# Kernel optimization log

Measured on AMD Instinct MI355X. Metric: run time of the kernel, lower is better.

Reference implementation:

```python
import jax, jax.numpy as jnp
import numpy as np

B, H, W, C = 4, 64, 64, 256
CP = C // 2  # downsize_factor = 2

def setup_inputs() -> dict:
    key = jax.random.key(0)
    ks = jax.random.split(key, 5)
    s = 1.0 / np.sqrt(C)
    return {
        "x": jax.random.normal(ks[0], (B, H, W, C), dtype=jnp.float32),
        "Wk": jax.random.normal(ks[1], (C, CP), dtype=jnp.float32) * s,
        "bk": jnp.zeros((CP,), dtype=jnp.float32),
        "Wq": jax.random.normal(ks[2], (C, CP), dtype=jnp.float32) * s,
        "bq": jnp.zeros((CP,), dtype=jnp.float32),
        "Wv": jax.random.normal(ks[3], (C, CP), dtype=jnp.float32) * s,
        "bv": jnp.zeros((CP,), dtype=jnp.float32),
        "Ws": jax.random.normal(ks[4], (C, CP), dtype=jnp.float32) * s,
        "bs": jnp.zeros((CP,), dtype=jnp.float32),
    }

def reference(x, Wk, bk, Wq, bq, Wv, bv, Ws, bs):
    b, h, w, c = x.shape
    n = h * w
    xf = x.reshape(b, n, c)  # 1x1 conv == per-pixel matmul
    K = xf @ Wk + bk  # [b, n, c']
    Q = xf @ Wq + bq  # [b, n, c']
    V = xf @ Wv + bv  # [b, n, c']
    # Keras Dot(axes=(2,1))([K, Q^T]) -> scores = K @ Q^T (no 1/sqrt(d) scaling)
    scores = jnp.einsum('bnc,bmc->bnm', K, Q)
    attn = jax.nn.softmax(scores, axis=-1)
    out = jnp.einsum('bnm,bmc->bnc', attn, V)  # [b, n, c']
    shortcut = xf @ Ws + bs  # downsize_factor > 1 path
    return (out + shortcut).reshape(b, h, w, out.shape[-1])
```

## Files before the change

kernel.cpp:

```cpp
#include <hip/hip_runtime.h>
#include <math.h>

typedef unsigned short u16;
typedef __attribute__((ext_vector_type(8))) _Float16 half8;
typedef __attribute__((ext_vector_type(4))) float    f32x4;

#define BATCH 4
#define NPB   4096
#define BN    16384
#define CC    256
#define D     128
#define LOG2E 1.44269504088896f
#define THR   8.0f

#if __has_builtin(__builtin_amdgcn_exp2f)
#define EXP2(x) __builtin_amdgcn_exp2f(x)
#else
#define EXP2(x) exp2f(x)
#endif

template<int CTRL>
__device__ __forceinline__ float dpp_mov(float x) {
    return __builtin_bit_cast(float, __builtin_amdgcn_update_dpp(
        __builtin_bit_cast(int, x), __builtin_bit_cast(int, x),
        CTRL, 0xf, 0xf, false));
}
__device__ __forceinline__ float dpp_row_max(float x) {
    x = fmaxf(x, dpp_mov<0x128>(x));
    x = fmaxf(x, dpp_mov<0x124>(x));
    x = fmaxf(x, dpp_mov<0x122>(x));
    x = fmaxf(x, dpp_mov<0x121>(x));
    return x;
}
__device__ __forceinline__ float dpp_row_sum(float x) {
    x += dpp_mov<0x128>(x);
    x += dpp_mov<0x124>(x);
    x += dpp_mov<0x122>(x);
    x += dpp_mov<0x121>(x);
    return x;
}

__global__ __launch_bounds__(256) void prep_kernel(
    const float* __restrict__ Wk, const float* __restrict__ Wq,
    const float* __restrict__ Wv, const float* __restrict__ Ws,
    u16* __restrict__ Wt)
{
    const int f   = (blockIdx.x * 256 + threadIdx.x) * 4;
    const int mat = f >> 15;
    const int rem = f & 32767;
    const int c   = rem >> 8;
    const int k0  = rem & 255;
    const float* W = (mat == 0) ? Wk : (mat == 1) ? Wq : (mat == 2) ? Wv : Ws;
    const float scale = (mat == 0) ? LOG2E : 1.0f;
    _Float16 t4[4];
#pragma unroll
    for (int i = 0; i < 4; ++i)
        t4[i] = (_Float16)(W[(size_t)(k0 + i) * D + c] * scale);
    *(uint2*)&Wt[(size_t)mat * 32768 + (size_t)c * 256 + k0] = *(const uint2*)t4;
}

#define APJ 264

__global__ __launch_bounds__(256, 2) void proj_kernel(
    const float* __restrict__ x, const u16* __restrict__ Wt,
    const float* __restrict__ bk, const float* __restrict__ bq,
    const float* __restrict__ bv, const float* __restrict__ bs,
    u16* __restrict__ Kh, u16* __restrict__ Qf,
    u16* __restrict__ Vf, float* __restrict__ Sc)
{
    __shared__ __align__(16) u16 As[128][APJ];

    const int tid = threadIdx.x;
    const int wv  = tid >> 6;
    const int l   = tid & 63;
    const int l15 = l & 15;
    const int l4  = l >> 4;
    const int by  = blockIdx.y;
    const int gm0 = blockIdx.x * 128;
    const int c0  = wv * 32;

    const u16* wb = Wt + (size_t)by * 32768 + (size_t)(c0 + l15) * 256 + l4 * 8;
    half8 wf[2][8];
#pragma unroll
    for (int ct = 0; ct < 2; ++ct)
#pragma unroll
        for (int kc = 0; kc < 8; ++kc)
            wf[ct][kc] = *(const half8*)(wb + ct * 16 * 256 + kc * 32);

    {
        const float4* xg = (const float4*)(x + (size_t)gm0 * CC);
#pragma unroll 8
        for (int i = 0; i < 32; ++i) {
            const int f = i * 256 + tid;
            const float4 v = xg[f];
            const int row = f >> 6, col4 = f & 63;
            _Float16 h[4] = {(_Float16)v.x, (_Float16)v.y,
                             (_Float16)v.z, (_Float16)v.w};
            *(uint2*)&As[row][col4 * 4] = *(const uint2*)h;
        }
    }
    __syncthreads();

    f32x4 acc[8][2];
#pragma unroll
    for (int mt = 0; mt < 8; ++mt) {
        acc[mt][0] = (f32x4){0.f, 0.f, 0.f, 0.f};
        acc[mt][1] = (f32x4){0.f, 0.f, 0.f, 0.f};
    }

    if (by == 2) {
        for (int kc = 0; kc < 8; ++kc)
#pragma unroll
            for (int mt = 0; mt < 8; ++mt) {
                const half8 a = *(const half8*)&As[mt * 16 + l15][kc * 32 + l4 * 8];
                acc[mt][0] = __builtin_amdgcn_mfma_f32_16x16x32_f16(a, wf[0][kc], acc[mt][0], 0, 0, 0);
                acc[mt][1] = __builtin_amdgcn_mfma_f32_16x16x32_f16(a, wf[1][kc], acc[mt][1], 0, 0, 0);
            }
        const float bb[2] = {bv[c0 + l15], bv[c0 + 16 + l15]};
        const int batch = gm0 >> 12;
        const int mb    = (gm0 & 4095) >> 5;
        u16* vbp = Vf + (size_t)batch * (D * NPB);
#pragma unroll
        for (int mt = 0; mt < 8; ++mt)
#pragma unroll
            for (int ct = 0; ct < 2; ++ct) {
                _Float16 t4[4];
#pragma unroll
                for (int r = 0; r < 4; ++r)
                    t4[r] = (_Float16)(acc[mt][ct][r] + bb[ct]);
                const int blk = (mb + (mt >> 1)) * 8 + wv * 2 + ct;
                const int off = blk * 512 + l15 * 32 + (mt & 1) * 16 + l4 * 4;
                *(uint2*)&vbp[off] = *(const uint2*)t4;
            }
    } else {
        for (int kc = 0; kc < 8; ++kc)
#pragma unroll
            for (int mt = 0; mt < 8; ++mt) {
                const half8 a = *(const half8*)&As[mt * 16 + l15][kc * 32 + l4 * 8];
                acc[mt][0] = __builtin_amdgcn_mfma_f32_16x16x32_f16(wf[0][kc], a, acc[mt][0], 0, 0, 0);
                acc[mt][1] = __builtin_amdgcn_mfma_f32_16x16x32_f16(wf[1][kc], a, acc[mt][1], 0, 0, 0);
            }
        if (by == 3) {
            float bb2[2][4];
#pragma unroll
            for (int ct = 0; ct < 2; ++ct)
#pragma unroll
                for (int r = 0; r < 4; ++r)
                    bb2[ct][r] = bs[c0 + ct * 16 + l4 * 4 + r];
#pragma unroll
            for (int mt = 0; mt < 8; ++mt) {
                const int m = gm0 + mt * 16 + l15;
#pragma unroll
                for (int ct = 0; ct < 2; ++ct) {
                    float4 v;
                    v.x = acc[mt][ct][0] + bb2[ct][0];
                    v.y = acc[mt][ct][1] + bb2[ct][1];
                    v.z = acc[mt][ct][2] + bb2[ct][2];
                    v.w = acc[mt][ct][3] + bb2[ct][3];
                    *(float4*)&Sc[(size_t)m * D + c0 + ct * 16 + l4 * 4] = v;
                }
            }
        } else if (by == 1) {
            float bb2[2][4];
#pragma unroll
            for (int ct = 0; ct < 2; ++ct)
#pragma unroll
                for (int r = 0; r < 4; ++r)
                    bb2[ct][r] = bq[c0 + ct * 16 + l4 * 4 + r];
#pragma unroll
            for (int mt = 0; mt < 8; ++mt) {
                const int blk = (((gm0 >> 4) + mt) << 2) + wv;
#pragma unroll
                for (int ct = 0; ct < 2; ++ct) {
                    _Float16 t4[4];
#pragma unroll
                    for (int r = 0; r < 4; ++r)
                        t4[r] = (_Float16)(acc[mt][ct][r] + bb2[ct][r]);
                    const int off = blk * 512 + (ct * 2 + (l4 >> 1)) * 128
                                    + l15 * 8 + (l4 & 1) * 4;
                    *(uint2*)&Qf[off] = *(const uint2*)t4;
                }
            }
        } else {
            float bb2[2][4];
#pragma unroll
            for (int ct = 0; ct < 2; ++ct)
#pragma unroll
                for (int r = 0; r < 4; ++r)
                    bb2[ct][r] = bk[c0 + ct * 16 + l4 * 4 + r] * LOG2E;
#pragma unroll
            for (int mt = 0; mt < 8; ++mt) {
                const int m = gm0 + mt * 16 + l15;
#pragma unroll
                for (int ct = 0; ct < 2; ++ct) {
                    _Float16 t4[4];
#pragma unroll
                    for (int r = 0; r < 4; ++r)
                        t4[r] = (_Float16)(acc[mt][ct][r] + bb2[ct][r]);
                    *(uint2*)&Kh[(size_t)m * D + c0 + ct * 16 + l4 * 4] =
                        *(const uint2*)t4;
                }
            }
        }
    }
}

#define VPP 40
#define OBP 132

__global__ __launch_bounds__(512, 2) void attn_kernel(
    const u16* __restrict__ Kh, const u16* __restrict__ Qf,
    const u16* __restrict__ Vf, const float* __restrict__ Sc,
    float* __restrict__ out)
{
    __shared__ __align__(16) unsigned char smem[4 * 16 * OBP * 4];
    __shared__ float ml[8][2][32];
    u16   (*Ps)[2][16][VPP] = (u16(*)[2][16][VPP])smem;
    float (*Obuf)[16][OBP]  = (float(*)[16][OBP])smem;

    const int tid = threadIdx.x;
    const int wv  = tid >> 6;
    const int l   = tid & 63;
    const int l15 = l & 15;
    const int l4  = l >> 4;

    const int bx    = blockIdx.x;
    const int xcd   = bx & 7;
    const int batch = xcd >> 1;
    const int tile  = ((xcd & 1) << 6) | (bx >> 3);
    const int gr0   = batch * NPB + tile * 32;

    half8 kf[2][4];
#pragma unroll
    for (int nt = 0; nt < 2; ++nt)
#pragma unroll
        for (int kc = 0; kc < 4; ++kc)
            kf[nt][kc] = *(const half8*)(
                Kh + (size_t)(gr0 + nt * 16 + l15) * D + kc * 32 + l4 * 8);

    const int  qtb = (batch * NPB + wv * 512) >> 4;
    const int  vbb = wv * 16;
    const u16* vb  = Vf + (size_t)batch * (D * NPB);
    const int  vl  = l15 * 4 + l4;

    f32x4 Oc[2][8];
#pragma unroll
    for (int nt = 0; nt < 2; ++nt)
#pragma unroll
        for (int ct = 0; ct < 8; ++ct)
            Oc[nt][ct] = (f32x4){0.f, 0.f, 0.f, 0.f};
    float mold[2][4], lsum[2][4];
#pragma unroll
    for (int nt = 0; nt < 2; ++nt)
#pragma unroll
        for (int r = 0; r < 4; ++r) { mold[nt][r] = -1e30f; lsum[nt][r] = 0.f; }

    for (int it = 0; it < 16; ++it) {
        half8 qf[2][4];
#pragma unroll
        for (int mt = 0; mt < 2; ++mt)
#pragma unroll
            for (int kc = 0; kc < 4; ++kc)
                qf[mt][kc] = *(const half8*)(
                    Qf + (size_t)(((qtb + it * 2 + mt) << 2) + kc) * 512 + l * 8);
        half8 vf[8];
#pragma unroll
        for (int ct = 0; ct < 8; ++ct)
            vf[ct] = *(const half8*)(
                vb + (size_t)(((vbb + it) << 3) + ct) * 512 + vl * 8);

        f32x4 sacc[2][2];
        sacc[0][0] = (f32x4){0.f, 0.f, 0.f, 0.f};
        sacc[0][1] = (f32x4){0.f, 0.f, 0.f, 0.f};
        sacc[1][0] = (f32x4){0.f, 0.f, 0.f, 0.f};
        sacc[1][1] = (f32x4){0.f, 0.f, 0.f, 0.f};
        __builtin_amdgcn_s_setprio(1);
#pragma unroll
        for (int kc = 0; kc < 4; ++kc)
#pragma unroll
            for (int nt = 0; nt < 2; ++nt)
#pragma unroll
                for (int mt = 0; mt < 2; ++mt)
                    sacc[nt][mt] = __builtin_amdgcn_mfma_f32_16x16x32_f16(
                        kf[nt][kc], qf[mt][kc], sacc[nt][mt], 0, 0, 0);
        __builtin_amdgcn_s_setprio(0);

        float rmax[2][4];
        int grow = 0;
#pragma unroll
        for (int nt = 0; nt < 2; ++nt)
#pragma unroll
            for (int r = 0; r < 4; ++r) {
                rmax[nt][r] = dpp_row_max(fmaxf(sacc[nt][0][r], sacc[nt][1][r]));
                grow |= (rmax[nt][r] > mold[nt][r] + THR) ? 1 : 0;
            }
        if (__any(grow)) {
#pragma unroll
            for (int nt = 0; nt < 2; ++nt)
#pragma unroll
                for (int r = 0; r < 4; ++r) {
                    const float mnew  = fmaxf(mold[nt][r], rmax[nt][r]);
                    const float alpha = EXP2(mold[nt][r] - mnew);
                    mold[nt][r] = mnew;
                    lsum[nt][r] *= alpha;
#pragma unroll
                    for (int ct = 0; ct < 8; ++ct) Oc[nt][ct][r] *= alpha;
                }
        }
#pragma unroll
        for (int nt = 0; nt < 2; ++nt)
#pragma unroll
            for (int r = 0; r < 4; ++r) {
                const float p0 = EXP2(sacc[nt][0][r] - mold[nt][r]);
                const float p1 = EXP2(sacc[nt][1][r] - mold[nt][r]);
                lsum[nt][r] += p0 + p1;
                Ps[wv][nt][l4 * 4 + r][l15]      = __builtin_bit_cast(u16, (_Float16)p0);
                Ps[wv][nt][l4 * 4 + r][16 + l15] = __builtin_bit_cast(u16, (_Float16)p1);
            }
        asm volatile("s_waitcnt lgkmcnt(0)" ::: "memory");

        __builtin_amdgcn_s_setprio(1);
#pragma unroll
        for (int nt = 0; nt < 2; ++nt) {
            const half8 pf = *(const half8*)&Ps[wv][nt][l15][l4 * 8];
#pragma unroll
            for (int ct = 0; ct < 8; ++ct)
                Oc[nt][ct] = __builtin_amdgcn_mfma_f32_16x16x32_f16(
                    pf, vf[ct], Oc[nt][ct], 0, 0, 0);
        }
        __builtin_amdgcn_s_setprio(0);
    }

#pragma unroll
    for (int nt = 0; nt < 2; ++nt)
#pragma unroll
        for (int r = 0; r < 4; ++r)
            lsum[nt][r] = dpp_row_sum(lsum[nt][r]);

    if (l15 == 0) {
#pragma unroll
        for (int nt = 0; nt < 2; ++nt)
#pragma unroll
            for (int r = 0; r < 4; ++r) {
                ml[wv][0][nt * 16 + l4 * 4 + r] = mold[nt][r];
                ml[wv][1][nt * 16 + l4 * 4 + r] = lsum[nt][r];
            }
    }
    __syncthreads();

    float fw[2][4];
#pragma unroll
    for (int nt = 0; nt < 2; ++nt)
#pragma unroll
        for (int r = 0; r < 4; ++r) {
            const int row = nt * 16 + l4 * 4 + r;
            float M = ml[0][0][row];
#pragma unroll
            for (int s = 1; s < 8; ++s) M = fmaxf(M, ml[s][0][row]);
            fw[nt][r] = EXP2(mold[nt][r] - M);
        }

#pragma unroll
    for (int nt = 0; nt < 2; ++nt) {
        if (wv >= 4) {
#pragma unroll
            for (int r = 0; r < 4; ++r) {
                const int row = l4 * 4 + r;
#pragma unroll
                for (int ct = 0; ct < 8; ++ct)
                    Obuf[wv - 4][row][ct * 16 + l15] = Oc[nt][ct][r] * fw[nt][r];
            }
        }
        __syncthreads();
        if (wv < 4) {
#pragma unroll
            for (int r = 0; r < 4; ++r) {
                const int row = l4 * 4 + r;
#pragma unroll
                for (int ct = 0; ct < 8; ++ct)
                    Obuf[wv][row][ct * 16 + l15] += Oc[nt][ct][r] * fw[nt][r];
            }
        }
        __syncthreads();

        {
            const int row  = tid >> 5;
            const int c    = (tid & 31) * 4;
            const int lrow = nt * 16 + row;
            float M = ml[0][0][lrow];
#pragma unroll
            for (int s = 1; s < 8; ++s) M = fmaxf(M, ml[s][0][lrow]);
            float L = 0.f;
#pragma unroll
            for (int s = 0; s < 8; ++s)
                L += ml[s][1][lrow] * EXP2(ml[s][0][lrow] - M);
            const float invL = 1.f / L;
            const size_t grow_ = (size_t)(gr0 + lrow);
            f32x4 a = *(const f32x4*)&Obuf[0][row][c];
#pragma unroll
            for (int s = 1; s < 4; ++s) {
                const f32x4 b = *(const f32x4*)&Obuf[s][row][c];
                a[0] += b[0]; a[1] += b[1]; a[2] += b[2]; a[3] += b[3];
            }
            const float4 sc = *(const float4*)&Sc[grow_ * D + c];
            float4 o;
            o.x = a[0] * invL + sc.x;
            o.y = a[1] * invL + sc.y;
            o.z = a[2] * invL + sc.z;
            o.w = a[3] * invL + sc.w;
            *(float4*)&out[grow_ * D + c] = o;
        }
        __syncthreads();
    }
}

extern "C" void kernel_launch(void* const* d_in, const int* in_sizes, int n_in,
                              void* d_out, int out_size, void* d_ws, size_t ws_size,
                              hipStream_t stream) {
    const float* x  = (const float*)d_in[0];
    const float* Wk = (const float*)d_in[1];
    const float* bk = (const float*)d_in[2];
    const float* Wq = (const float*)d_in[3];
    const float* bq = (const float*)d_in[4];
    const float* Wv = (const float*)d_in[5];
    const float* bv = (const float*)d_in[6];
    const float* Ws = (const float*)d_in[7];
    const float* bs = (const float*)d_in[8];
    float* out = (float*)d_out;

    u16*   Kh = (u16*)d_ws;
    u16*   Qf = Kh + (size_t)BN * D;
    u16*   Vf = Qf + (size_t)BN * D;
    float* Sc = (float*)(Vf + (size_t)BN * D);
    u16*   Wt = (u16*)(Sc + (size_t)BN * D);

    prep_kernel<<<128, 256, 0, stream>>>(Wk, Wq, Wv, Ws, Wt);
    proj_kernel<<<dim3(128, 4), 256, 0, stream>>>(x, Wt, bk, bq, bv, bs,
                                                  Kh, Qf, Vf, Sc);
    attn_kernel<<<512, 512, 0, stream>>>(Kh, Qf, Vf, Sc, out);
}
```

Measured before the change: 163.6 us.

## Double attention row tile to 64 per block with K staged in LDS

Each attention block now handles 64 query rows instead of 32, so every Q and V fragment loaded from global memory is reused across four row tiles instead of two. This halves the total Q/V traffic across the grid. K rows are staged in shared memory and read per MFMA rather than held in registers, to offset the larger accumulator footprint. Launch bounds drop to one block per CU and the grid halves to 256 blocks, which risks lower occupancy, extra register pressure and added LDS reads.

```diff
diff --git a/kernel.cpp b/kernel.cpp
--- a/kernel.cpp
+++ b/kernel.cpp
@@ -207,15 +207,17 @@
 
 #define VPP 40
 #define OBP 132
-
-__global__ __launch_bounds__(512, 2) void attn_kernel(
+#define KSP 136
+
+__global__ __launch_bounds__(512, 1) void attn_kernel(
     const u16* __restrict__ Kh, const u16* __restrict__ Qf,
     const u16* __restrict__ Vf, const float* __restrict__ Sc,
     float* __restrict__ out)
 {
-    __shared__ __align__(16) unsigned char smem[4 * 16 * OBP * 4];
-    __shared__ float ml[8][2][32];
-    u16   (*Ps)[2][16][VPP] = (u16(*)[2][16][VPP])smem;
+    __shared__ __align__(16) u16 Ks[64][KSP];
+    __shared__ __align__(16) unsigned char smem[8 * 4 * 16 * VPP * 2];
+    __shared__ float ml[8][2][64];
+    u16   (*Ps)[4][16][VPP] = (u16(*)[4][16][VPP])smem;
     float (*Obuf)[16][OBP]  = (float(*)[16][OBP])smem;
 
     const int tid = threadIdx.x;
@@ -227,31 +229,31 @@
     const int bx    = blockIdx.x;
     const int xcd   = bx & 7;
     const int batch = xcd >> 1;
-    const int tile  = ((xcd & 1) << 6) | (bx >> 3);
-    const int gr0   = batch * NPB + tile * 32;
-
-    half8 kf[2][4];
-#pragma unroll
-    for (int nt = 0; nt < 2; ++nt)
-#pragma unroll
-        for (int kc = 0; kc < 4; ++kc)
-            kf[nt][kc] = *(const half8*)(
-                Kh + (size_t)(gr0 + nt * 16 + l15) * D + kc * 32 + l4 * 8);
+    const int tile  = ((xcd & 1) << 5) | (bx >> 3);
+    const int gr0   = batch * NPB + tile * 64;
+
+    {
+        const int row = tid >> 3, ch = tid & 7;
+        const uint4* src = (const uint4*)(Kh + (size_t)(gr0 + row) * D + ch * 16);
+        *(uint4*)&Ks[row][ch * 16]     = src[0];
+        *(uint4*)&Ks[row][ch * 16 + 8] = src[1];
+    }
+    __syncthreads();
 
     const int  qtb = (batch * NPB + wv * 512) >> 4;
     const int  vbb = wv * 16;
     const u16* vb  = Vf + (size_t)batch * (D * NPB);
     const int  vl  = l15 * 4 + l4;
 
-    f32x4 Oc[2][8];
-#pragma unroll
-    for (int nt = 0; nt < 2; ++nt)
+    f32x4 Oc[4][8];
+#pragma unroll
+    for (int nt = 0; nt < 4; ++nt)
 #pragma unroll
         for (int ct = 0; ct < 8; ++ct)
             Oc[nt][ct] = (f32x4){0.f, 0.f, 0.f, 0.f};
-    float mold[2][4], lsum[2][4];
-#pragma unroll
-    for (int nt = 0; nt < 2; ++nt)
+    float mold[4][4], lsum[4][4];
+#pragma unroll
+    for (int nt = 0; nt < 4; ++nt)
 #pragma unroll
         for (int r = 0; r < 4; ++r) { mold[nt][r] = -1e30f; lsum[nt][r] = 0.f; }
 
@@ -269,26 +271,30 @@
             vf[ct] = *(const half8*)(
                 vb + (size_t)(((vbb + it) << 3) + ct) * 512 + vl * 8);
 
-        f32x4 sacc[2][2];
-        sacc[0][0] = (f32x4){0.f, 0.f, 0.f, 0.f};
-        sacc[0][1] = (f32x4){0.f, 0.f, 0.f, 0.f};
-        sacc[1][0] = (f32x4){0.f, 0.f, 0.f, 0.f};
-        sacc[1][1] = (f32x4){0.f, 0.f, 0.f, 0.f};
+        f32x4 sacc[4][2];
+#pragma unroll
+        for (int nt = 0; nt < 4; ++nt) {
+            sacc[nt][0] = (f32x4){0.f, 0.f, 0.f, 0.f};
+            sacc[nt][1] = (f32x4){0.f, 0.f, 0.f, 0.f};
+        }
         __builtin_amdgcn_s_setprio(1);
 #pragma unroll
         for (int kc = 0; kc < 4; ++kc)
 #pragma unroll
-            for (int nt = 0; nt < 2; ++nt)
+            for (int nt = 0; nt < 4; ++nt) {
+                const half8 kfr =
+                    *(const half8*)&Ks[nt * 16 + l15][kc * 32 + l4 * 8];
 #pragma unroll
                 for (int mt = 0; mt < 2; ++mt)
                     sacc[nt][mt] = __builtin_amdgcn_mfma_f32_16x16x32_f16(
-                        kf[nt][kc], qf[mt][kc], sacc[nt][mt], 0, 0, 0);
+                        kfr, qf[mt][kc], sacc[nt][mt], 0, 0, 0);
+            }
         __builtin_amdgcn_s_setprio(0);
 
-        float rmax[2][4];
+        float rmax[4][4];
         int grow = 0;
 #pragma unroll
-        for (int nt = 0; nt < 2; ++nt)
+        for (int nt = 0; nt < 4; ++nt)
 #pragma unroll
             for (int r = 0; r < 4; ++r) {
                 rmax[nt][r] = dpp_row_max(fmaxf(sacc[nt][0][r], sacc[nt][1][r]));
@@ -296,7 +302,7 @@
             }
         if (__any(grow)) {
 #pragma unroll
-            for (int nt = 0; nt < 2; ++nt)
+            for (int nt = 0; nt < 4; ++nt)
 #pragma unroll
                 for (int r = 0; r < 4; ++r) {
                     const float mnew  = fmaxf(mold[nt][r], rmax[nt][r]);
@@ -308,7 +314,7 @@
                 }
         }
 #pragma unroll
-        for (int nt = 0; nt < 2; ++nt)
+        for (int nt = 0; nt < 4; ++nt)
 #pragma unroll
             for (int r = 0; r < 4; ++r) {
                 const float p0 = EXP2(sacc[nt][0][r] - mold[nt][r]);
@@ -321,7 +327,7 @@
 
         __builtin_amdgcn_s_setprio(1);
 #pragma unroll
-        for (int nt = 0; nt < 2; ++nt) {
+        for (int nt = 0; nt < 4; ++nt) {
             const half8 pf = *(const half8*)&Ps[wv][nt][l15][l4 * 8];
 #pragma unroll
             for (int ct = 0; ct < 8; ++ct)
@@ -332,14 +338,14 @@
     }
 
 #pragma unroll
-    for (int nt = 0; nt < 2; ++nt)
+    for (int nt = 0; nt < 4; ++nt)
 #pragma unroll
         for (int r = 0; r < 4; ++r)
             lsum[nt][r] = dpp_row_sum(lsum[nt][r]);
 
     if (l15 == 0) {
 #pragma unroll
-        for (int nt = 0; nt < 2; ++nt)
+        for (int nt = 0; nt < 4; ++nt)
 #pragma unroll
             for (int r = 0; r < 4; ++r) {
                 ml[wv][0][nt * 16 + l4 * 4 + r] = mold[nt][r];
@@ -348,9 +354,9 @@
     }
     __syncthreads();
 
-    float fw[2][4];
-#pragma unroll
-    for (int nt = 0; nt < 2; ++nt)
+    float fw[4][4];
+#pragma unroll
+    for (int nt = 0; nt < 4; ++nt)
 #pragma unroll
         for (int r = 0; r < 4; ++r) {
             const int row = nt * 16 + l4 * 4 + r;
@@ -361,7 +367,7 @@
         }
 
 #pragma unroll
-    for (int nt = 0; nt < 2; ++nt) {
+    for (int nt = 0; nt < 4; ++nt) {
         if (wv >= 4) {
 #pragma unroll
             for (int r = 0; r < 4; ++r) {
@@ -437,5 +443,5 @@
     prep_kernel<<<128, 256, 0, stream>>>(Wk, Wq, Wv, Ws, Wt);
     proj_kernel<<<dim3(128, 4), 256, 0, stream>>>(x, Wt, bk, bq, bv, bs,
                                                   Kh, Qf, Vf, Sc);
-    attn_kernel<<<512, 512, 0, stream>>>(Kh, Qf, Vf, Sc, out);
-}
+    attn_kernel<<<256, 512, 0, stream>>>(Kh, Qf, Vf, Sc, out);
+}
```

Result: no change. 161.0 us (-1.6%).
